# Optimization experiments

Hardware: AMD Instinct MI355X
Metric: run time of the kernel (lower is better)

## Reference

```python
import jax, jax.numpy as jnp
import numpy as np

EPSILON = 1e-7  # wl-coref utils.add_dummy epsilon
LEAKY_SLOPE = 0.01  # torch.nn.LeakyReLU default

N_MENTIONS = 10000
BATCH = 512
N_ANTS = 50
MENTION_EMB = 1024
PW_EMB = 64
IN_FEATURES = 3 * MENTION_EMB + PW_EMB  # 3136
HIDDEN = 128


def setup_inputs() -> dict:
    key = jax.random.key(0)
    ks = jax.random.split(key, 9)
    return {
        "all_mentions": jax.random.normal(ks[0], (N_MENTIONS, MENTION_EMB), jnp.float32),
        "mentions_batch": jax.random.normal(ks[1], (BATCH, MENTION_EMB), jnp.float32),
        "pw_batch": jax.random.normal(ks[2], (BATCH, N_ANTS, PW_EMB), jnp.float32),
        "top_indices_batch": jax.random.randint(ks[3], (BATCH, N_ANTS), 0, N_MENTIONS, jnp.int64 if jax.config.jax_enable_x64 else jnp.int32),
        "top_rough_scores_batch": jax.random.normal(ks[4], (BATCH, N_ANTS), jnp.float32),
        "W1": jax.random.normal(ks[5], (IN_FEATURES, HIDDEN), jnp.float32) * 0.02,
        "b1": jax.random.normal(ks[6], (HIDDEN,), jnp.float32) * 0.02,
        "W_out": jax.random.normal(ks[7], (HIDDEN, 1), jnp.float32) * 0.02,
        "b_out": jax.random.normal(ks[8], (1,), jnp.float32) * 0.02,
    }


def reference(all_mentions, mentions_batch, pw_batch, top_indices_batch,
              top_rough_scores_batch, W1, b1, W_out, b_out):
    batch, n_ants = top_indices_batch.shape
    emb = mentions_batch.shape[1]
    # pair matrix: [batch, n_ants, 3*emb + pw_emb]
    a_mentions = jnp.broadcast_to(mentions_batch[:, None, :], (batch, n_ants, emb))
    b_mentions = all_mentions[top_indices_batch]          # gather: [batch, n_ants, emb]
    similarity = a_mentions * b_mentions
    pair_matrix = jnp.concatenate((a_mentions, b_mentions, similarity, pw_batch), axis=2)
    # FFNN: Linear -> LeakyReLU -> (Dropout=identity in eval) -> Linear(out=1)
    h = jax.nn.leaky_relu(jnp.einsum('baf,fh->bah', pair_matrix, W1) + b1, LEAKY_SLOPE)
    ffnn = (jnp.einsum('bah,ho->bao', h, W_out) + b_out)[..., 0]  # [batch, n_ants]
    scores = top_rough_scores_batch + ffnn
    # add_dummy(eps=True): prepend a column of EPSILON
    dummy = jnp.full((batch, 1), EPSILON, dtype=scores.dtype)
    return jnp.concatenate((dummy, scores), axis=1)  # [batch, n_ants + 1]
```

## Files before the change

kernel.cpp:

```cpp
#include <hip/hip_runtime.h>

#define N_MENT   10000
#define BATCH    512
#define N_ANTS   50
#define EMB      1024
#define PW_EMB   64
#define IN_F     3136
#define HID      128
#define M_TOT    (BATCH * N_ANTS)
#define EPS_VAL  1e-7f
#define SLOPE    0.01f
#define NKT      98

using f32x4 = __attribute__((ext_vector_type(4))) float;
using s16x8 = __attribute__((ext_vector_type(8))) short;
using u16x8 = __attribute__((ext_vector_type(8))) unsigned short;

__device__ __forceinline__ unsigned short f2bf(float f) {
  unsigned u = __builtin_bit_cast(unsigned, f);
  u += 0x7FFFu + ((u >> 16) & 1u);
  return (unsigned short)(u >> 16);
}

__global__ __launch_bounds__(256) void k_convert(const float* __restrict__ w1,
                                                 unsigned short* __restrict__ w1f) {
  const int id   = blockIdx.x * 256 + threadIdx.x;
  const int lane = id & 63;
  const int tile = id >> 6;
  const int tk   = tile % NKT, tn = tile / NKT;
  const int n    = tn * 16 + (lane & 15);
  const int k    = tk * 32 + (lane >> 4) * 8;
  u16x8 o;
  #pragma unroll
  for (int j = 0; j < 8; ++j) o[j] = f2bf(w1[(size_t)(k + j) * HID + n]);
  *(u16x8*)(w1f + (size_t)id * 8) = o;
}

__global__ __launch_bounds__(256) void k_amab(const float* __restrict__ all_m,
                                              const float* __restrict__ men,
                                              const unsigned short* __restrict__ w1f,
                                              float* __restrict__ amab) {
  __shared__ __align__(16) unsigned short Xs[2][32 * 72];

  const int t   = threadIdx.x;
  const int bid = blockIdx.x;
  const bool isAM   = (bid < 16);
  const int base    = isAM ? bid * 32 : (bid - 16) * 32;
  const int nrows   = isAM ? BATCH : N_MENT;
  const int tkbase  = isAM ? 0 : 32;
  const float* src  = isAM ? men : all_m;
  const int outbase = isAM ? base : BATCH + base;

  const int sr = t >> 3, sq = t & 7;
  const int srow = (base + sr < nrows) ? base + sr : nrows - 1;
  const float* pX = src + (size_t)srow * EMB + sq * 8;

  const int lane = t & 63, wid = t >> 6;
  const int ln = lane & 15, lg = lane >> 4;
  const int wcol = wid * 32;
  const unsigned short* wf0 = w1f + (((size_t)(wid * 2)     * NKT) * 64 + lane) * 8;
  const unsigned short* wf1 = w1f + (((size_t)(wid * 2 + 1) * NKT) * 64 + lane) * 8;

  f32x4 acc[2][2] = {};

  float4 r0 = ((const float4*)pX)[0];
  float4 r1 = ((const float4*)pX)[1];
  s16x8 bc00 = *(const s16x8*)(wf0 + (size_t)(tkbase)     * 512);
  s16x8 bc01 = *(const s16x8*)(wf1 + (size_t)(tkbase)     * 512);
  s16x8 bc10 = *(const s16x8*)(wf0 + (size_t)(tkbase + 1) * 512);
  s16x8 bc11 = *(const s16x8*)(wf1 + (size_t)(tkbase + 1) * 512);

  int buf = 0;
  for (int s = 0; s < 16; ++s) {
    u16x8 px;
    px[0]=f2bf(r0.x); px[1]=f2bf(r0.y); px[2]=f2bf(r0.z); px[3]=f2bf(r0.w);
    px[4]=f2bf(r1.x); px[5]=f2bf(r1.y); px[6]=f2bf(r1.z); px[7]=f2bf(r1.w);
    *(u16x8*)&Xs[buf][sr * 72 + sq * 8] = px;

    if (s < 15) {
      const float* q = pX + (s + 1) * 64;
      r0 = ((const float4*)q)[0];
      r1 = ((const float4*)q)[1];
    }
    const int tkn = tkbase + (s < 15 ? (s + 1) : s) * 2;
    s16x8 bn00 = *(const s16x8*)(wf0 + (size_t)(tkn)     * 512);
    s16x8 bn01 = *(const s16x8*)(wf1 + (size_t)(tkn)     * 512);
    s16x8 bn10 = *(const s16x8*)(wf0 + (size_t)(tkn + 1) * 512);
    s16x8 bn11 = *(const s16x8*)(wf1 + (size_t)(tkn + 1) * 512);

    __syncthreads();
    #pragma unroll
    for (int mf = 0; mf < 2; ++mf) {
      s16x8 a0 = *(const s16x8*)&Xs[buf][(mf * 16 + ln) * 72 + lg * 8];
      s16x8 a1 = *(const s16x8*)&Xs[buf][(mf * 16 + ln) * 72 + 32 + lg * 8];
      acc[mf][0] = __builtin_amdgcn_mfma_f32_16x16x32_bf16(a0, bc00, acc[mf][0], 0, 0, 0);
      acc[mf][1] = __builtin_amdgcn_mfma_f32_16x16x32_bf16(a0, bc01, acc[mf][1], 0, 0, 0);
      acc[mf][0] = __builtin_amdgcn_mfma_f32_16x16x32_bf16(a1, bc10, acc[mf][0], 0, 0, 0);
      acc[mf][1] = __builtin_amdgcn_mfma_f32_16x16x32_bf16(a1, bc11, acc[mf][1], 0, 0, 0);
    }
    bc00 = bn00; bc01 = bn01; bc10 = bn10; bc11 = bn11;
    buf ^= 1;
  }
  #pragma unroll
  for (int mf = 0; mf < 2; ++mf)
    #pragma unroll
    for (int e = 0; e < 4; ++e) {
      const int r = mf * 16 + lg * 4 + e;
      if (base + r < nrows) {
        amab[(size_t)(outbase + r) * HID + wcol + ln]      = acc[mf][0][e];
        amab[(size_t)(outbase + r) * HID + wcol + 16 + ln] = acc[mf][1][e];
      }
    }
}

__global__ __launch_bounds__(256) void k_main(const float* __restrict__ all_m,
                                              const float* __restrict__ men,
                                              const float* __restrict__ pw,
                                              const int*   __restrict__ topi,
                                              const float* __restrict__ rough,
                                              const unsigned short* __restrict__ w1f,
                                              const float* __restrict__ amab,
                                              const float* __restrict__ b1,
                                              const float* __restrict__ wout,
                                              const float* __restrict__ bout,
                                              float* __restrict__ out) {
  __shared__ __align__(16) unsigned short Xs[2][32 * 72];
  __shared__ float red[4 * 32];

  const int t  = threadIdx.x;
  const int m0 = blockIdx.x * 32;

  const int sr = t >> 3, sq = t & 7;
  const int m  = m0 + sr;
  const int bb = m / N_ANTS;
  const int bidx = topi[m];
  const float* pA = men   + (size_t)bb   * EMB    + sq * 8;
  const float* pB = all_m + (size_t)bidx * EMB    + sq * 8;
  const float* pP = pw    + (size_t)m    * PW_EMB + sq * 8;

  const int lane = t & 63, wid = t >> 6;
  const int ln = lane & 15, lg = lane >> 4;
  const int wcol = wid * 32;
  const unsigned short* wf0 = w1f + (((size_t)(wid * 2)     * NKT) * 64 + lane) * 8;
  const unsigned short* wf1 = w1f + (((size_t)(wid * 2 + 1) * NKT) * 64 + lane) * 8;

  f32x4 acc[2][2] = {};

  float4 ra0 = ((const float4*)pA)[0];
  float4 ra1 = ((const float4*)pA)[1];
  float4 rb0 = ((const float4*)pB)[0];
  float4 rb1 = ((const float4*)pB)[1];
  s16x8 bc00 = *(const s16x8*)(wf0 + (size_t)(64)     * 512);
  s16x8 bc01 = *(const s16x8*)(wf1 + (size_t)(64)     * 512);
  s16x8 bc10 = *(const s16x8*)(wf0 + (size_t)(64 + 1) * 512);
  s16x8 bc11 = *(const s16x8*)(wf1 + (size_t)(64 + 1) * 512);

  int buf = 0;
  for (int s = 0; s < 17; ++s) {
    u16x8 px;
    px[0]=f2bf(ra0.x*rb0.x); px[1]=f2bf(ra0.y*rb0.y);
    px[2]=f2bf(ra0.z*rb0.z); px[3]=f2bf(ra0.w*rb0.w);
    px[4]=f2bf(ra1.x*rb1.x); px[5]=f2bf(ra1.y*rb1.y);
    px[6]=f2bf(ra1.z*rb1.z); px[7]=f2bf(ra1.w*rb1.w);
    *(u16x8*)&Xs[buf][sr * 72 + sq * 8] = px;

    if (s < 15) {
      const float* qA = pA + (s + 1) * 64;
      const float* qB = pB + (s + 1) * 64;
      ra0 = ((const float4*)qA)[0]; ra1 = ((const float4*)qA)[1];
      rb0 = ((const float4*)qB)[0]; rb1 = ((const float4*)qB)[1];
    } else if (s == 15) {
      ra0 = ((const float4*)pP)[0];  ra1 = ((const float4*)pP)[1];
      rb0 = make_float4(1.f, 1.f, 1.f, 1.f); rb1 = rb0;
    }
    const int tkn = 64 + (s < 16 ? (s + 1) : s) * 2;
    s16x8 bn00 = *(const s16x8*)(wf0 + (size_t)(tkn)     * 512);
    s16x8 bn01 = *(const s16x8*)(wf1 + (size_t)(tkn)     * 512);
    s16x8 bn10 = *(const s16x8*)(wf0 + (size_t)(tkn + 1) * 512);
    s16x8 bn11 = *(const s16x8*)(wf1 + (size_t)(tkn + 1) * 512);

    __syncthreads();
    #pragma unroll
    for (int mf = 0; mf < 2; ++mf) {
      s16x8 a0 = *(const s16x8*)&Xs[buf][(mf * 16 + ln) * 72 + lg * 8];
      s16x8 a1 = *(const s16x8*)&Xs[buf][(mf * 16 + ln) * 72 + 32 + lg * 8];
      acc[mf][0] = __builtin_amdgcn_mfma_f32_16x16x32_bf16(a0, bc00, acc[mf][0], 0, 0, 0);
      acc[mf][1] = __builtin_amdgcn_mfma_f32_16x16x32_bf16(a0, bc01, acc[mf][1], 0, 0, 0);
      acc[mf][0] = __builtin_amdgcn_mfma_f32_16x16x32_bf16(a1, bc10, acc[mf][0], 0, 0, 0);
      acc[mf][1] = __builtin_amdgcn_mfma_f32_16x16x32_bf16(a1, bc11, acc[mf][1], 0, 0, 0);
    }
    bc00 = bn00; bc01 = bn01; bc10 = bn10; bc11 = bn11;
    buf ^= 1;
  }

  const int n0 = wcol + ln, n1 = wcol + 16 + ln;
  const float bias0 = b1[n0], bias1 = b1[n1];
  const float w_0 = wout[n0], w_1 = wout[n1];
  #pragma unroll
  for (int mf = 0; mf < 2; ++mf)
    #pragma unroll
    for (int e = 0; e < 4; ++e) {
      const int ml = mf * 16 + lg * 4 + e;
      const int gm = m0 + ml;
      const int gb = gm / N_ANTS;
      const int gi = topi[gm];
      const float* amr = amab + (size_t)gb * HID;
      const float* abr = amab + (size_t)(BATCH + gi) * HID;
      float h0 = acc[mf][0][e] + amr[n0] + abr[n0] + bias0;
      float h1 = acc[mf][1][e] + amr[n1] + abr[n1] + bias1;
      h0 = h0 > 0.f ? h0 : SLOPE * h0;
      h1 = h1 > 0.f ? h1 : SLOPE * h1;
      float ss = h0 * w_0 + h1 * w_1;
      ss += __shfl_xor(ss, 1);
      ss += __shfl_xor(ss, 2);
      ss += __shfl_xor(ss, 4);
      ss += __shfl_xor(ss, 8);
      if (ln == 0) red[wid * 32 + ml] = ss;
    }
  __syncthreads();
  if (t < 32) {
    const int gm = m0 + t;
    const int gb = gm / N_ANTS;
    const int ga = gm - gb * N_ANTS;
    out[(size_t)gb * (N_ANTS + 1) + 1 + ga] =
        rough[gm] + red[t] + red[32 + t] + red[64 + t] + red[96 + t] + bout[0];
  }
  if (t == 0) {
    for (int g = m0 / N_ANTS; g <= (m0 + 31) / N_ANTS; ++g)
      out[(size_t)g * (N_ANTS + 1)] = EPS_VAL;
  }
}

__global__ void k_eps(float* __restrict__ out) {
  out[(size_t)threadIdx.x * (N_ANTS + 1)] = EPS_VAL;
}

__global__ __launch_bounds__(128) void k_fb(const float* __restrict__ all_m,
                                            const float* __restrict__ men,
                                            const float* __restrict__ pw,
                                            const int*   __restrict__ topi,
                                            const float* __restrict__ rough,
                                            const float* __restrict__ w1,
                                            const float* __restrict__ b1,
                                            const float* __restrict__ wout,
                                            const float* __restrict__ bout,
                                            float* __restrict__ out) {
  __shared__ float xs[IN_F];
  __shared__ float hred[HID];
  const int pair = blockIdx.x;
  const int t = threadIdx.x;
  const int bb = pair / N_ANTS;
  const int idx = topi[pair];
  const float* pA = men + (size_t)bb * EMB;
  const float* pB = all_m + (size_t)idx * EMB;
  for (int k = t; k < EMB; k += 128) {
    float a = pA[k], b = pB[k];
    xs[k] = a; xs[EMB + k] = b; xs[2 * EMB + k] = a * b;
  }
  if (t < PW_EMB) xs[3 * EMB + t] = pw[(size_t)pair * PW_EMB + t];
  __syncthreads();
  float acc = 0.f;
  for (int k = 0; k < IN_F; ++k) acc = fmaf(xs[k], w1[(size_t)k * HID + t], acc);
  acc += b1[t];
  acc = acc > 0.f ? acc : SLOPE * acc;
  hred[t] = acc * wout[t];
  __syncthreads();
  for (int off = 64; off > 0; off >>= 1) {
    if (t < off) hred[t] += hred[t + off];
    __syncthreads();
  }
  if (t == 0)
    out[(size_t)bb * (N_ANTS + 1) + 1 + (pair - bb * N_ANTS)] = rough[pair] + hred[0] + bout[0];
}

extern "C" void kernel_launch(void* const* d_in, const int* in_sizes, int n_in,
                              void* d_out, int out_size, void* d_ws, size_t ws_size,
                              hipStream_t stream) {
  const float* all_m = (const float*)d_in[0];
  const float* men   = (const float*)d_in[1];
  const float* pw    = (const float*)d_in[2];
  const int*   topi  = (const int*)  d_in[3];
  const float* rough = (const float*)d_in[4];
  const float* w1    = (const float*)d_in[5];
  const float* b1    = (const float*)d_in[6];
  const float* wout  = (const float*)d_in[7];
  const float* bout  = (const float*)d_in[8];
  float* out = (float*)d_out;

  const size_t W1F_BYTES  = (size_t)HID * IN_F * sizeof(unsigned short);
  const size_t AMAB_BYTES = (size_t)(BATCH + N_MENT) * HID * sizeof(float);

  if (ws_size >= W1F_BYTES + AMAB_BYTES) {
    unsigned short* w1f = (unsigned short*)d_ws;
    float* amab = (float*)((char*)d_ws + W1F_BYTES);
    k_convert<<<196, 256, 0, stream>>>(w1, w1f);
    k_amab<<<16 + (N_MENT + 31) / 32, 256, 0, stream>>>(all_m, men, w1f, amab);
    k_main<<<M_TOT / 32, 256, 0, stream>>>(all_m, men, pw, topi, rough, w1f, amab,
                                           b1, wout, bout, out);
  } else {
    k_eps<<<1, BATCH, 0, stream>>>(out);
    k_fb<<<M_TOT, 128, 0, stream>>>(all_m, men, pw, topi, rough, w1, b1, wout, bout, out);
  }
}
```

Measured before the change: 52.71 us.

## Fuse amab and main kernels with atomic counter dependency and packed bf16 conversion

Merges the precompute kernel (mention-row projections) and the main pair-scoring kernel into one launch. Main blocks run their similarity GEMM first, then spin on a global counter until every precompute block has published its results, so the two phases can overlap and one launch boundary goes away. Also swaps the manual bf16 rounding for the hardware v_cvt_pk_bf16_f32 instruction and adds an occupancy hint of 5 blocks per CU. The spin-wait depends on the precompute blocks being scheduled ahead of the waiting blocks, which adds a small deadlock risk and an extra memset call.

```diff
diff --git a/kernel.cpp b/kernel.cpp
--- a/kernel.cpp
+++ b/kernel.cpp
@@ -12,6 +12,11 @@
 #define SLOPE    0.01f
 #define NKT      98
 
+#define AMAB_ROWS  (BATCH + N_MENT)
+#define AMAB_BLK   (16 + (N_MENT + 31) / 32)
+#define MAIN_BLK   (M_TOT / 32)
+#define TOT_BLK    (AMAB_BLK + MAIN_BLK)
+
 using f32x4 = __attribute__((ext_vector_type(4))) float;
 using s16x8 = __attribute__((ext_vector_type(8))) short;
 using u16x8 = __attribute__((ext_vector_type(8))) unsigned short;
@@ -20,6 +25,15 @@
   unsigned u = __builtin_bit_cast(unsigned, f);
   u += 0x7FFFu + ((u >> 16) & 1u);
   return (unsigned short)(u >> 16);
+}
+
+__device__ __forceinline__ u16x8 pack8(float4 lo, float4 hi) {
+  union { u16x8 v; unsigned u[4]; } r;
+  asm("v_cvt_pk_bf16_f32 %0, %1, %2" : "=v"(r.u[0]) : "v"(lo.x), "v"(lo.y));
+  asm("v_cvt_pk_bf16_f32 %0, %1, %2" : "=v"(r.u[1]) : "v"(lo.z), "v"(lo.w));
+  asm("v_cvt_pk_bf16_f32 %0, %1, %2" : "=v"(r.u[2]) : "v"(hi.x), "v"(hi.y));
+  asm("v_cvt_pk_bf16_f32 %0, %1, %2" : "=v"(r.u[3]) : "v"(hi.z), "v"(hi.w));
+  return r.v;
 }
 
 __global__ __launch_bounds__(256) void k_convert(const float* __restrict__ w1,
@@ -36,113 +50,97 @@
   *(u16x8*)(w1f + (size_t)id * 8) = o;
 }
 
-__global__ __launch_bounds__(256) void k_amab(const float* __restrict__ all_m,
-                                              const float* __restrict__ men,
-                                              const unsigned short* __restrict__ w1f,
-                                              float* __restrict__ amab) {
+__global__ __launch_bounds__(256, 5) void k_fused(
+    const float* __restrict__ all_m, const float* __restrict__ men,
+    const float* __restrict__ pw, const int* __restrict__ topi,
+    const float* __restrict__ rough, const unsigned short* __restrict__ w1f,
+    float* __restrict__ amab, const float* __restrict__ b1,
+    const float* __restrict__ wout, const float* __restrict__ bout,
+    float* __restrict__ out, unsigned* __restrict__ cnt) {
   __shared__ __align__(16) unsigned short Xs[2][32 * 72];
-
-  const int t   = threadIdx.x;
-  const int bid = blockIdx.x;
-  const bool isAM   = (bid < 16);
-  const int base    = isAM ? bid * 32 : (bid - 16) * 32;
-  const int nrows   = isAM ? BATCH : N_MENT;
-  const int tkbase  = isAM ? 0 : 32;
-  const float* src  = isAM ? men : all_m;
-  const int outbase = isAM ? base : BATCH + base;
-
-  const int sr = t >> 3, sq = t & 7;
-  const int srow = (base + sr < nrows) ? base + sr : nrows - 1;
-  const float* pX = src + (size_t)srow * EMB + sq * 8;
-
+  __shared__ float red[4 * 32];
+
+  const int t    = threadIdx.x;
+  const int bid  = blockIdx.x;
   const int lane = t & 63, wid = t >> 6;
-  const int ln = lane & 15, lg = lane >> 4;
+  const int ln   = lane & 15, lg = lane >> 4;
   const int wcol = wid * 32;
   const unsigned short* wf0 = w1f + (((size_t)(wid * 2)     * NKT) * 64 + lane) * 8;
   const unsigned short* wf1 = w1f + (((size_t)(wid * 2 + 1) * NKT) * 64 + lane) * 8;
-
-  f32x4 acc[2][2] = {};
-
-  float4 r0 = ((const float4*)pX)[0];
-  float4 r1 = ((const float4*)pX)[1];
-  s16x8 bc00 = *(const s16x8*)(wf0 + (size_t)(tkbase)     * 512);
-  s16x8 bc01 = *(const s16x8*)(wf1 + (size_t)(tkbase)     * 512);
-  s16x8 bc10 = *(const s16x8*)(wf0 + (size_t)(tkbase + 1) * 512);
-  s16x8 bc11 = *(const s16x8*)(wf1 + (size_t)(tkbase + 1) * 512);
-
-  int buf = 0;
-  for (int s = 0; s < 16; ++s) {
-    u16x8 px;
-    px[0]=f2bf(r0.x); px[1]=f2bf(r0.y); px[2]=f2bf(r0.z); px[3]=f2bf(r0.w);
-    px[4]=f2bf(r1.x); px[5]=f2bf(r1.y); px[6]=f2bf(r1.z); px[7]=f2bf(r1.w);
-    *(u16x8*)&Xs[buf][sr * 72 + sq * 8] = px;
-
-    if (s < 15) {
-      const float* q = pX + (s + 1) * 64;
-      r0 = ((const float4*)q)[0];
-      r1 = ((const float4*)q)[1];
+  const int sr = t >> 3, sq = t & 7;
+
+  if (bid < AMAB_BLK) {
+    const bool isAM   = (bid < 16);
+    const int base    = isAM ? bid * 32 : (bid - 16) * 32;
+    const int nrows   = isAM ? BATCH : N_MENT;
+    const int tkbase  = isAM ? 0 : 32;
+    const float* src  = isAM ? men : all_m;
+    const int outbase = isAM ? base : BATCH + base;
+
+    const int srow = (base + sr < nrows) ? base + sr : nrows - 1;
+    const float* pX = src + (size_t)srow * EMB + sq * 8;
+
+    f32x4 acc[2][2] = {};
+    float4 r0 = ((const float4*)pX)[0];
+    float4 r1 = ((const float4*)pX)[1];
+    s16x8 bc00 = *(const s16x8*)(wf0 + (size_t)(tkbase)     * 512);
+    s16x8 bc01 = *(const s16x8*)(wf1 + (size_t)(tkbase)     * 512);
+    s16x8 bc10 = *(const s16x8*)(wf0 + (size_t)(tkbase + 1) * 512);
+    s16x8 bc11 = *(const s16x8*)(wf1 + (size_t)(tkbase + 1) * 512);
+
+    int buf = 0;
+    for (int s = 0; s < 16; ++s) {
+      *(u16x8*)&Xs[buf][sr * 72 + sq * 8] = pack8(r0, r1);
+      if (s < 15) {
+        const float* q = pX + (s + 1) * 64;
+        r0 = ((const float4*)q)[0];
+        r1 = ((const float4*)q)[1];
+      }
+      const int tkn = tkbase + (s < 15 ? (s + 1) : s) * 2;
+      s16x8 bn00 = *(const s16x8*)(wf0 + (size_t)(tkn)     * 512);
+      s16x8 bn01 = *(const s16x8*)(wf1 + (size_t)(tkn)     * 512);
+      s16x8 bn10 = *(const s16x8*)(wf0 + (size_t)(tkn + 1) * 512);
+      s16x8 bn11 = *(const s16x8*)(wf1 + (size_t)(tkn + 1) * 512);
+
+      __syncthreads();
+      #pragma unroll
+      for (int mf = 0; mf < 2; ++mf) {
+        s16x8 a0 = *(const s16x8*)&Xs[buf][(mf * 16 + ln) * 72 + lg * 8];
+        s16x8 a1 = *(const s16x8*)&Xs[buf][(mf * 16 + ln) * 72 + 32 + lg * 8];
+        acc[mf][0] = __builtin_amdgcn_mfma_f32_16x16x32_bf16(a0, bc00, acc[mf][0], 0, 0, 0);
+        acc[mf][1] = __builtin_amdgcn_mfma_f32_16x16x32_bf16(a0, bc01, acc[mf][1], 0, 0, 0);
+        acc[mf][0] = __builtin_amdgcn_mfma_f32_16x16x32_bf16(a1, bc10, acc[mf][0], 0, 0, 0);
+        acc[mf][1] = __builtin_amdgcn_mfma_f32_16x16x32_bf16(a1, bc11, acc[mf][1], 0, 0, 0);
+      }
+      bc00 = bn00; bc01 = bn01; bc10 = bn10; bc11 = bn11;
+      buf ^= 1;
     }
-    const int tkn = tkbase + (s < 15 ? (s + 1) : s) * 2;
-    s16x8 bn00 = *(const s16x8*)(wf0 + (size_t)(tkn)     * 512);
-    s16x8 bn01 = *(const s16x8*)(wf1 + (size_t)(tkn)     * 512);
-    s16x8 bn10 = *(const s16x8*)(wf0 + (size_t)(tkn + 1) * 512);
-    s16x8 bn11 = *(const s16x8*)(wf1 + (size_t)(tkn + 1) * 512);
-
+    #pragma unroll
+    for (int mf = 0; mf < 2; ++mf)
+      #pragma unroll
+      for (int e = 0; e < 4; ++e) {
+        const int r = mf * 16 + lg * 4 + e;
+        if (base + r < nrows) {
+          amab[(size_t)(outbase + r) * HID + wcol + ln]      = acc[mf][0][e];
+          amab[(size_t)(outbase + r) * HID + wcol + 16 + ln] = acc[mf][1][e];
+        }
+      }
+    __threadfence();
     __syncthreads();
-    #pragma unroll
-    for (int mf = 0; mf < 2; ++mf) {
-      s16x8 a0 = *(const s16x8*)&Xs[buf][(mf * 16 + ln) * 72 + lg * 8];
-      s16x8 a1 = *(const s16x8*)&Xs[buf][(mf * 16 + ln) * 72 + 32 + lg * 8];
-      acc[mf][0] = __builtin_amdgcn_mfma_f32_16x16x32_bf16(a0, bc00, acc[mf][0], 0, 0, 0);
-      acc[mf][1] = __builtin_amdgcn_mfma_f32_16x16x32_bf16(a0, bc01, acc[mf][1], 0, 0, 0);
-      acc[mf][0] = __builtin_amdgcn_mfma_f32_16x16x32_bf16(a1, bc10, acc[mf][0], 0, 0, 0);
-      acc[mf][1] = __builtin_amdgcn_mfma_f32_16x16x32_bf16(a1, bc11, acc[mf][1], 0, 0, 0);
-    }
-    bc00 = bn00; bc01 = bn01; bc10 = bn10; bc11 = bn11;
-    buf ^= 1;
-  }
-  #pragma unroll
-  for (int mf = 0; mf < 2; ++mf)
-    #pragma unroll
-    for (int e = 0; e < 4; ++e) {
-      const int r = mf * 16 + lg * 4 + e;
-      if (base + r < nrows) {
-        amab[(size_t)(outbase + r) * HID + wcol + ln]      = acc[mf][0][e];
-        amab[(size_t)(outbase + r) * HID + wcol + 16 + ln] = acc[mf][1][e];
-      }
-    }
-}
-
-__global__ __launch_bounds__(256) void k_main(const float* __restrict__ all_m,
-                                              const float* __restrict__ men,
-                                              const float* __restrict__ pw,
-                                              const int*   __restrict__ topi,
-                                              const float* __restrict__ rough,
-                                              const unsigned short* __restrict__ w1f,
-                                              const float* __restrict__ amab,
-                                              const float* __restrict__ b1,
-                                              const float* __restrict__ wout,
-                                              const float* __restrict__ bout,
-                                              float* __restrict__ out) {
-  __shared__ __align__(16) unsigned short Xs[2][32 * 72];
-  __shared__ float red[4 * 32];
-
-  const int t  = threadIdx.x;
-  const int m0 = blockIdx.x * 32;
-
-  const int sr = t >> 3, sq = t & 7;
+    if (t == 0)
+      __hip_atomic_fetch_add(&cnt[0], 1u, __ATOMIC_RELEASE, __HIP_MEMORY_SCOPE_AGENT);
+    return;
+  }
+
+  const int mb = bid - AMAB_BLK;
+  const int m0 = mb * 32;
+
   const int m  = m0 + sr;
   const int bb = m / N_ANTS;
   const int bidx = topi[m];
   const float* pA = men   + (size_t)bb   * EMB    + sq * 8;
   const float* pB = all_m + (size_t)bidx * EMB    + sq * 8;
   const float* pP = pw    + (size_t)m    * PW_EMB + sq * 8;
-
-  const int lane = t & 63, wid = t >> 6;
-  const int ln = lane & 15, lg = lane >> 4;
-  const int wcol = wid * 32;
-  const unsigned short* wf0 = w1f + (((size_t)(wid * 2)     * NKT) * 64 + lane) * 8;
-  const unsigned short* wf1 = w1f + (((size_t)(wid * 2 + 1) * NKT) * 64 + lane) * 8;
 
   f32x4 acc[2][2] = {};
 
@@ -157,12 +155,9 @@
 
   int buf = 0;
   for (int s = 0; s < 17; ++s) {
-    u16x8 px;
-    px[0]=f2bf(ra0.x*rb0.x); px[1]=f2bf(ra0.y*rb0.y);
-    px[2]=f2bf(ra0.z*rb0.z); px[3]=f2bf(ra0.w*rb0.w);
-    px[4]=f2bf(ra1.x*rb1.x); px[5]=f2bf(ra1.y*rb1.y);
-    px[6]=f2bf(ra1.z*rb1.z); px[7]=f2bf(ra1.w*rb1.w);
-    *(u16x8*)&Xs[buf][sr * 72 + sq * 8] = px;
+    float4 plo = make_float4(ra0.x * rb0.x, ra0.y * rb0.y, ra0.z * rb0.z, ra0.w * rb0.w);
+    float4 phi = make_float4(ra1.x * rb1.x, ra1.y * rb1.y, ra1.z * rb1.z, ra1.w * rb1.w);
+    *(u16x8*)&Xs[buf][sr * 72 + sq * 8] = pack8(plo, phi);
 
     if (s < 15) {
       const float* qA = pA + (s + 1) * 64;
@@ -192,6 +187,13 @@
     bc00 = bn00; bc01 = bn01; bc10 = bn10; bc11 = bn11;
     buf ^= 1;
   }
+
+  if (t == 0) {
+    while (__hip_atomic_load(&cnt[0], __ATOMIC_ACQUIRE, __HIP_MEMORY_SCOPE_AGENT)
+           < (unsigned)AMAB_BLK)
+      __builtin_amdgcn_s_sleep(2);
+  }
+  __syncthreads();
 
   const int n0 = wcol + ln, n1 = wcol + 16 + ln;
   const float bias0 = b1[n0], bias1 = b1[n1];
@@ -287,16 +289,18 @@
   const float* bout  = (const float*)d_in[8];
   float* out = (float*)d_out;
 
+  const size_t CNT_BYTES  = 256;
   const size_t W1F_BYTES  = (size_t)HID * IN_F * sizeof(unsigned short);
-  const size_t AMAB_BYTES = (size_t)(BATCH + N_MENT) * HID * sizeof(float);
-
-  if (ws_size >= W1F_BYTES + AMAB_BYTES) {
-    unsigned short* w1f = (unsigned short*)d_ws;
-    float* amab = (float*)((char*)d_ws + W1F_BYTES);
+  const size_t AMAB_BYTES = (size_t)AMAB_ROWS * HID * sizeof(float);
+
+  if (ws_size >= CNT_BYTES + W1F_BYTES + AMAB_BYTES) {
+    unsigned* cnt = (unsigned*)d_ws;
+    unsigned short* w1f = (unsigned short*)((char*)d_ws + CNT_BYTES);
+    float* amab = (float*)((char*)d_ws + CNT_BYTES + W1F_BYTES);
+    hipMemsetAsync(d_ws, 0, 8, stream);
     k_convert<<<196, 256, 0, stream>>>(w1, w1f);
-    k_amab<<<16 + (N_MENT + 31) / 32, 256, 0, stream>>>(all_m, men, w1f, amab);
-    k_main<<<M_TOT / 32, 256, 0, stream>>>(all_m, men, pw, topi, rough, w1f, amab,
-                                           b1, wout, bout, out);
+    k_fused<<<TOT_BLK, 256, 0, stream>>>(all_m, men, pw, topi, rough, w1f, amab,
+                                         b1, wout, bout, out, cnt);
   } else {
     k_eps<<<1, BATCH, 0, stream>>>(out);
     k_fb<<<M_TOT, 128, 0, stream>>>(all_m, men, pw, topi, rough, w1, b1, wout, bout, out);
```

After: 101.8 us. 1.93x slower.
